# Kernel optimization log

Measured on AMD Instinct MI355X. Metric: run time of the kernel, lower is better.

Reference implementation:

```python
import jax, jax.numpy as jnp
import numpy as np

N_LETTERS = 256
EMBED_DIM = 1024
HIDDEN_DIM = 2048
SEQ_LEN = 4096


def setup_inputs() -> dict:
    key = jax.random.key(0)
    ks = jax.random.split(key, 8)
    s_e = 1.0 / np.sqrt(EMBED_DIM)
    s_h = 1.0 / np.sqrt(HIDDEN_DIM)
    return {
        "input_ids": jax.random.randint(ks[0], (SEQ_LEN,), 0, N_LETTERS, dtype=jnp.int64)
        if jax.config.jax_enable_x64 else jax.random.randint(ks[0], (SEQ_LEN,), 0, N_LETTERS, dtype=jnp.int32),
        "h0": jnp.zeros((1, 1, HIDDEN_DIM), jnp.float32),
        "c0": jnp.zeros((1, 1, HIDDEN_DIM), jnp.float32),
        "W_emb": jax.random.normal(ks[1], (N_LETTERS, EMBED_DIM), jnp.float32),
        "W_ih": jax.random.normal(ks[2], (4 * HIDDEN_DIM, EMBED_DIM), jnp.float32) * s_e,
        "W_hh": jax.random.normal(ks[3], (4 * HIDDEN_DIM, HIDDEN_DIM), jnp.float32) * s_h,
        "b_ih": jnp.zeros((4 * HIDDEN_DIM,), jnp.float32),
        "b_hh": jnp.zeros((4 * HIDDEN_DIM,), jnp.float32),
        "W_out": jax.random.normal(ks[4], (N_LETTERS, HIDDEN_DIM), jnp.float32) * s_h,
        "b_out": jnp.zeros((N_LETTERS,), jnp.float32),
    }


def reference(input_ids, h0, c0, W_emb, W_ih, W_hh, b_ih, b_hh, W_out, b_out):
    H = W_hh.shape[1]
    emb = W_emb[input_ids]                       # [L, E]
    # Precompute the input-side gate projections for all timesteps (batched GEMM).
    x_gates = emb @ W_ih.T + (b_ih + b_hh)       # [L, 4H]

    def step(carry, xg):
        h, c = carry                             # [H], [H]
        gates = xg + W_hh @ h                    # [4H], PyTorch order i,f,g,o
        i = jax.nn.sigmoid(gates[0 * H:1 * H])
        f = jax.nn.sigmoid(gates[1 * H:2 * H])
        g = jnp.tanh(gates[2 * H:3 * H])
        o = jax.nn.sigmoid(gates[3 * H:4 * H])
        c_new = f * c + i * g
        h_new = o * jnp.tanh(c_new)
        return (h_new, c_new), h_new

    (hL, cL), hs = jax.lax.scan(step, (h0[0, 0], c0[0, 0]), x_gates)  # hs: [L, H]
    logits = hs @ W_out.T + b_out                # [L, n_letters]
    # Dropout(p=0.1) is identity in eval mode.
    out = jax.nn.log_softmax(jax.nn.relu(logits), axis=-1)
    return out, hL[None, None, :], cL[None, None, :]
```

## Files before the change

### kernel.cpp

```cpp
#include <hip/hip_runtime.h>
#include <hip/hip_bf16.h>

#define SEQ 4096
#define EMB 1024
#define HID 2048
#define G4  8192
#define NL  256

typedef __attribute__((ext_vector_type(8))) short bf16x8;
typedef __attribute__((ext_vector_type(4))) float f32x4;

static __device__ __forceinline__ unsigned short f2bf(float f) {
    unsigned int x = __builtin_bit_cast(unsigned int, f);
    return (unsigned short)((x + 0x7FFFu + ((x >> 16) & 1u)) >> 16);
}
static __device__ __forceinline__ float bf2f(unsigned short u) {
    return __builtin_bit_cast(float, ((unsigned int)u) << 16);
}
static __device__ __forceinline__ unsigned long long aload(const unsigned long long* p) {
    return __hip_atomic_load(p, __ATOMIC_RELAXED, __HIP_MEMORY_SCOPE_AGENT);
}
static __device__ __forceinline__ float fsigm(float x) {
    return 1.f / (1.f + __expf(-x));
}
static __device__ __forceinline__ float ftanh(float x) {
    return 1.f - 2.f / (__expf(2.f * x) + 1.f);
}

__global__ __launch_bounds__(256) void k_f2b(const float* __restrict__ in,
                                             unsigned short* __restrict__ out, int n) {
    int i = (blockIdx.x * 256 + threadIdx.x) * 4;
    if (i < n) {
        float4 v = *(const float4*)&in[i];
        ushort4 u;
        u.x = f2bf(v.x); u.y = f2bf(v.y); u.z = f2bf(v.z); u.w = f2bf(v.w);
        *(ushort4*)&out[i] = u;
    }
}

__global__ __launch_bounds__(256) void k_emb(const int* __restrict__ ids,
                                             const float* __restrict__ W_emb,
                                             unsigned short* __restrict__ out) {
    int t = blockIdx.x;
    int e0 = threadIdx.x * 4;
    const float4 v = *(const float4*)&W_emb[(size_t)ids[t] * EMB + e0];
    ushort4 u;
    u.x = f2bf(v.x); u.y = f2bf(v.y); u.z = f2bf(v.z); u.w = f2bf(v.w);
    *(ushort4*)&out[(size_t)t * EMB + e0] = u;
}

#define BM 128
#define BN 128
#define BK 32
__global__ __launch_bounds__(256) void k_gemm_bt(
    const unsigned short* __restrict__ A, const unsigned short* __restrict__ B,
    const float* __restrict__ bias1, const float* __restrict__ bias2,
    float* __restrict__ Cf, unsigned short* __restrict__ Cb,
    int M, int N, int K)
{
    __shared__ unsigned short As[BM * BK];
    __shared__ unsigned short Bs[BN * BK];
    const int bm = blockIdx.x * BM;
    const int bn = blockIdx.y * BN;
    const int tid = threadIdx.x;
    const int wave = tid >> 6, lane = tid & 63;
    const int wm = (wave & 1) * 64, wn = (wave >> 1) * 64;
    const int row16 = lane & 15, quad = lane >> 4;

    f32x4 acc[4][4];
#pragma unroll
    for (int i = 0; i < 4; ++i)
#pragma unroll
        for (int j = 0; j < 4; ++j) acc[i][j] = (f32x4){0.f, 0.f, 0.f, 0.f};

    for (int k0 = 0; k0 < K; k0 += BK) {
        __syncthreads();
#pragma unroll
        for (int s = 0; s < 2; ++s) {
            int c = tid + s * 256;
            int r = c >> 2, col = (c & 3) * 8;
            *(uint4*)&As[r * BK + col] = *(const uint4*)&A[(size_t)(bm + r) * K + k0 + col];
            *(uint4*)&Bs[r * BK + col] = *(const uint4*)&B[(size_t)(bn + r) * K + k0 + col];
        }
        __syncthreads();
        bf16x8 af[4], bfr[4];
#pragma unroll
        for (int i = 0; i < 4; ++i) {
            af[i]  = *(const bf16x8*)&As[(wm + i * 16 + row16) * BK + quad * 8];
            bfr[i] = *(const bf16x8*)&Bs[(wn + i * 16 + row16) * BK + quad * 8];
        }
#pragma unroll
        for (int i = 0; i < 4; ++i)
#pragma unroll
            for (int j = 0; j < 4; ++j)
                acc[i][j] = __builtin_amdgcn_mfma_f32_16x16x32_bf16(af[i], bfr[j], acc[i][j], 0, 0, 0);
    }

#pragma unroll
    for (int j = 0; j < 4; ++j) {
        int col = bn + wn + j * 16 + row16;
        float bsum = (bias1 ? bias1[col] : 0.f) + (bias2 ? bias2[col] : 0.f);
#pragma unroll
        for (int i = 0; i < 4; ++i) {
#pragma unroll
            for (int r = 0; r < 4; ++r) {
                int row = bm + wm + i * 16 + quad * 4 + r;
                float v = acc[i][j][r] + bsum;
                if (Cf) Cf[(size_t)row * N + col] = v;
                else    Cb[(size_t)row * N + col] = f2bf(v);
            }
        }
    }
}

#define LSTM_LDS 90112
__global__ __launch_bounds__(1024, 1) void k_lstm(
    const unsigned short* __restrict__ Whhb,
    const unsigned short* __restrict__ xg,
    const float* __restrict__ h0, const float* __restrict__ c0,
    unsigned short* __restrict__ hsb,
    float* __restrict__ outHC,
    unsigned long long* __restrict__ hcomm)
{
    extern __shared__ char smem[];
    float* LDSp = (float*)smem;

    const int b = blockIdx.x, tid = threadIdx.x;
    const int wave = tid >> 6, lane = tid & 63;
    const int sub = lane & 15, quad = lane >> 4;

    const int qa = (sub >> 3), qb = 2 + (sub >> 3), j = sub & 7;
    const unsigned short* wa = Whhb + ((size_t)(qa * HID + b * 8 + j)) * HID + wave * 128 + quad * 8;
    const unsigned short* wb = Whhb + ((size_t)(qb * HID + b * 8 + j)) * HID + wave * 128 + quad * 8;
    bf16x8 afrA[4], afrB[4];
#pragma unroll
    for (int c = 0; c < 4; ++c) {
        afrA[c] = *(const bf16x8*)(wa + c * 32);
        afrB[c] = *(const bf16x8*)(wb + c * 32);
    }

    float creg = 0.f;
    if (tid < 8) creg = c0[b * 8 + tid];

    for (int t = 0; t < SEQ; ++t) {
        float xq0 = 0.f, xq1 = 0.f, xq2 = 0.f, xq3 = 0.f;
        if (wave == 0 && lane < 8) {
            const unsigned short* xr = xg + (size_t)t * G4 + b * 8 + lane;
            xq0 = bf2f(xr[0]);
            xq1 = bf2f(xr[2048]);
            xq2 = bf2f(xr[4096]);
            xq3 = bf2f(xr[6144]);
        }

        f32x4 acc0 = (f32x4){0.f, 0.f, 0.f, 0.f};
        f32x4 acc1 = (f32x4){0.f, 0.f, 0.f, 0.f};

        if (t == 0) {
#pragma unroll
            for (int c = 0; c < 4; ++c) {
                const float* hp = h0 + wave * 128 + c * 32 + quad * 8;
                float4 va = *(const float4*)hp;
                float4 vb = *(const float4*)(hp + 4);
                uint4 d;
                d.x = (unsigned)f2bf(va.x) | ((unsigned)f2bf(va.y) << 16);
                d.y = (unsigned)f2bf(va.z) | ((unsigned)f2bf(va.w) << 16);
                d.z = (unsigned)f2bf(vb.x) | ((unsigned)f2bf(vb.y) << 16);
                d.w = (unsigned)f2bf(vb.z) | ((unsigned)f2bf(vb.w) << 16);
                bf16x8 hf = __builtin_bit_cast(bf16x8, d);
                acc0 = __builtin_amdgcn_mfma_f32_16x16x32_bf16(afrA[c], hf, acc0, 0, 0, 0);
                acc1 = __builtin_amdgcn_mfma_f32_16x16x32_bf16(afrB[c], hf, acc1, 0, 0, 0);
            }
        } else {
            const unsigned long long* src =
                hcomm + (size_t)((t - 1) & 1) * 8192 + (size_t)(b & 7) * 1024 + wave * 64;
            const unsigned tag = (unsigned)t;
            unsigned long long x;
            for (;;) {
                x = aload(&src[lane]);
                if ((unsigned)(x >> 32) == tag) break;
                __builtin_amdgcn_s_sleep(1);
            }
            int myd = (int)(unsigned)x;
#pragma unroll
            for (int c = 0; c < 4; ++c) {
                const int sl = c * 16 + quad * 4;
                uint4 d;
                d.x = (unsigned)__shfl(myd, sl + 0);
                d.y = (unsigned)__shfl(myd, sl + 1);
                d.z = (unsigned)__shfl(myd, sl + 2);
                d.w = (unsigned)__shfl(myd, sl + 3);
                bf16x8 hf = __builtin_bit_cast(bf16x8, d);
                acc0 = __builtin_amdgcn_mfma_f32_16x16x32_bf16(afrA[c], hf, acc0, 0, 0, 0);
                acc1 = __builtin_amdgcn_mfma_f32_16x16x32_bf16(afrB[c], hf, acc1, 0, 0, 0);
            }
        }

        float* P = LDSp + (t & 1) * 640;
        if (sub == 0) {
#pragma unroll
            for (int r = 0; r < 4; ++r) {
                P[(quad * 4 + r) * 20 + wave]      = acc0[r];
                P[(16 + quad * 4 + r) * 20 + wave] = acc1[r];
            }
        }
        __syncthreads();

        if (wave == 0) {
            float g = 0.f;
            if (lane < 32) {
                const float* rp = P + lane * 20;
                f32x4 s = *(const f32x4*)rp;
                s += *(const f32x4*)(rp + 4);
                s += *(const f32x4*)(rp + 8);
                s += *(const f32x4*)(rp + 12);
                g = s[0] + s[1] + s[2] + s[3];
            }
            float gF = __shfl(g, 8 + lane);
            float gG = __shfl(g, 16 + lane);
            float gO = __shfl(g, 24 + lane);
            unsigned hv = 0;
            float cn = 0.f, hn = 0.f;
            if (lane < 8) {
                float gi = g  + xq0;
                float gf = gF + xq1;
                float gg = gG + xq2;
                float go = gO + xq3;
                float i_ = fsigm(gi);
                float f_ = fsigm(gf);
                float g_ = ftanh(gg);
                float o_ = fsigm(go);
                cn = f_ * creg + i_ * g_;
                hn = o_ * ftanh(cn);
                creg = cn;
                hv = (unsigned)f2bf(hn);
            }
            {
                int jj = lane & 3;
                unsigned lo = (unsigned)__shfl((int)hv, 2 * jj);
                unsigned hi = (unsigned)__shfl((int)hv, 2 * jj + 1);
                if (lane < 32) {
                    unsigned long long wrd =
                        (((unsigned long long)(unsigned)(t + 1)) << 32)
                        | (unsigned long long)(lo | (hi << 16));
                    __hip_atomic_store(
                        &hcomm[(size_t)(t & 1) * 8192 + (size_t)(lane >> 2) * 1024 + b * 4 + jj],
                        wrd, __ATOMIC_RELAXED, __HIP_MEMORY_SCOPE_AGENT);
                }
            }
            if (lane < 8) {
                hsb[(size_t)t * HID + b * 8 + lane] = (unsigned short)hv;
                if (t == SEQ - 1) {
                    outHC[b * 8 + lane] = hn;
                    outHC[HID + b * 8 + lane] = cn;
                }
            }
        }
    }
}

__global__ __launch_bounds__(256) void k_softmax(const float* __restrict__ logits,
                                                 float* __restrict__ out) {
    int row = blockIdx.x * 4 + (threadIdx.x >> 6);
    int lane = threadIdx.x & 63;
    const float* Lr = logits + (size_t)row * NL;
    float4 v = *(const float4*)&Lr[lane * 4];
    v.x = fmaxf(v.x, 0.f); v.y = fmaxf(v.y, 0.f);
    v.z = fmaxf(v.z, 0.f); v.w = fmaxf(v.w, 0.f);
    float m = fmaxf(fmaxf(v.x, v.y), fmaxf(v.z, v.w));
#pragma unroll
    for (int off = 32; off > 0; off >>= 1) m = fmaxf(m, __shfl_xor(m, off));
    float e = __expf(v.x - m) + __expf(v.y - m) + __expf(v.z - m) + __expf(v.w - m);
#pragma unroll
    for (int off = 32; off > 0; off >>= 1) e += __shfl_xor(e, off);
    float ls = __logf(e) + m;
    float4 o;
    o.x = v.x - ls; o.y = v.y - ls; o.z = v.z - ls; o.w = v.w - ls;
    *(float4*)&out[(size_t)row * NL + lane * 4] = o;
}

extern "C" void kernel_launch(void* const* d_in, const int* in_sizes, int n_in,
                              void* d_out, int out_size, void* d_ws, size_t ws_size,
                              hipStream_t stream) {
    const int*   ids   = (const int*)d_in[0];
    const float* h0    = (const float*)d_in[1];
    const float* c0    = (const float*)d_in[2];
    const float* W_emb = (const float*)d_in[3];
    const float* W_ih  = (const float*)d_in[4];
    const float* W_hh  = (const float*)d_in[5];
    const float* b_ih  = (const float*)d_in[6];
    const float* b_hh  = (const float*)d_in[7];
    const float* W_out = (const float*)d_in[8];
    const float* b_out = (const float*)d_in[9];
    float* out = (float*)d_out;

    char* ws = (char*)d_ws;
    unsigned short* xg    = (unsigned short*)(ws);
    unsigned short* hsb   = (unsigned short*)(ws + 67108864);
    unsigned short* Wihb  = (unsigned short*)(ws + 83886080);
    unsigned short* embb  = (unsigned short*)(ws + 100663296);
    unsigned short* Woutb = (unsigned short*)(ws + 109051904);
    float*          logit = (float*)(ws + 110100480);
    unsigned short* Whhb  = (unsigned short*)(ws + 114294784);
    unsigned long long* hcomm = (unsigned long long*)(ws + 147849216);

    k_f2b<<<(G4 * EMB / 4 + 255) / 256, 256, 0, stream>>>(W_ih, Wihb, G4 * EMB);
    k_f2b<<<(NL * HID / 4 + 255) / 256, 256, 0, stream>>>(W_out, Woutb, NL * HID);
    k_f2b<<<(G4 * HID / 4 + 255) / 256, 256, 0, stream>>>(W_hh, Whhb, G4 * HID);
    k_emb<<<SEQ, 256, 0, stream>>>(ids, W_emb, embb);

    dim3 g1(SEQ / BM, G4 / BN);
    k_gemm_bt<<<g1, 256, 0, stream>>>(embb, Wihb, b_ih, b_hh, nullptr, xg, SEQ, G4, EMB);

    hipFuncSetAttribute((const void*)k_lstm, hipFuncAttributeMaxDynamicSharedMemorySize, LSTM_LDS);
    k_lstm<<<256, 1024, LSTM_LDS, stream>>>(Whhb, xg, h0, c0, hsb, out + (size_t)SEQ * NL, hcomm);

    dim3 g2(SEQ / BM, NL / BN);
    k_gemm_bt<<<g2, 256, 0, stream>>>(hsb, Woutb, b_out, nullptr, logit, nullptr, SEQ, NL, HID);

    k_softmax<<<SEQ / 4, 256, 0, stream>>>(logit, out);
}
```

Measured before the change: 10.69 ms.

## Halve LSTM grid so each block owns 16 hidden units with full MFMA tiles

The persistent LSTM kernel now runs 128 blocks, each owning 16 hidden units, instead of 256 blocks owning 8. Each wave holds all four gates' W_hh fragments in registers and issues four MFMAs per K-chunk, so every 16-row MFMA tile carries useful rows. The LDS partial-sum layout, the gate reduction, the hcomm broadcast packing and the c/h bookkeeping are reworked to match. Polling is also retuned: non-leader waves sleep before spinning and the spin sleep is longer. The aim is to cut per-step grid-wide synchronisation and polling contention by halving the number of participants. In exchange, each block does twice the matrix work per step and uses more registers.

```diff
diff --git a/kernel.cpp b/kernel.cpp
--- a/kernel.cpp
+++ b/kernel.cpp
@@ -129,31 +129,32 @@
     const int wave = tid >> 6, lane = tid & 63;
     const int sub = lane & 15, quad = lane >> 4;
 
-    const int qa = (sub >> 3), qb = 2 + (sub >> 3), j = sub & 7;
-    const unsigned short* wa = Whhb + ((size_t)(qa * HID + b * 8 + j)) * HID + wave * 128 + quad * 8;
-    const unsigned short* wb = Whhb + ((size_t)(qb * HID + b * 8 + j)) * HID + wave * 128 + quad * 8;
-    bf16x8 afrA[4], afrB[4];
-#pragma unroll
-    for (int c = 0; c < 4; ++c) {
-        afrA[c] = *(const bf16x8*)(wa + c * 32);
-        afrB[c] = *(const bf16x8*)(wb + c * 32);
+    bf16x8 afr[4][4];
+#pragma unroll
+    for (int q = 0; q < 4; ++q) {
+        const unsigned short* wsrc =
+            Whhb + ((size_t)(q * HID + b * 16 + sub)) * HID + wave * 128 + quad * 8;
+#pragma unroll
+        for (int c = 0; c < 4; ++c)
+            afr[q][c] = *(const bf16x8*)(wsrc + c * 32);
     }
 
     float creg = 0.f;
-    if (tid < 8) creg = c0[b * 8 + tid];
+    if (tid < 16) creg = c0[b * 16 + tid];
 
     for (int t = 0; t < SEQ; ++t) {
         float xq0 = 0.f, xq1 = 0.f, xq2 = 0.f, xq3 = 0.f;
-        if (wave == 0 && lane < 8) {
-            const unsigned short* xr = xg + (size_t)t * G4 + b * 8 + lane;
+        if (wave == 0 && lane < 16) {
+            const unsigned short* xr = xg + (size_t)t * G4 + b * 16 + lane;
             xq0 = bf2f(xr[0]);
             xq1 = bf2f(xr[2048]);
             xq2 = bf2f(xr[4096]);
             xq3 = bf2f(xr[6144]);
         }
 
-        f32x4 acc0 = (f32x4){0.f, 0.f, 0.f, 0.f};
-        f32x4 acc1 = (f32x4){0.f, 0.f, 0.f, 0.f};
+        f32x4 acc[4];
+#pragma unroll
+        for (int q = 0; q < 4; ++q) acc[q] = (f32x4){0.f, 0.f, 0.f, 0.f};
 
         if (t == 0) {
 #pragma unroll
@@ -167,18 +168,20 @@
                 d.z = (unsigned)f2bf(vb.x) | ((unsigned)f2bf(vb.y) << 16);
                 d.w = (unsigned)f2bf(vb.z) | ((unsigned)f2bf(vb.w) << 16);
                 bf16x8 hf = __builtin_bit_cast(bf16x8, d);
-                acc0 = __builtin_amdgcn_mfma_f32_16x16x32_bf16(afrA[c], hf, acc0, 0, 0, 0);
-                acc1 = __builtin_amdgcn_mfma_f32_16x16x32_bf16(afrB[c], hf, acc1, 0, 0, 0);
+#pragma unroll
+                for (int q = 0; q < 4; ++q)
+                    acc[q] = __builtin_amdgcn_mfma_f32_16x16x32_bf16(afr[q][c], hf, acc[q], 0, 0, 0);
             }
         } else {
             const unsigned long long* src =
                 hcomm + (size_t)((t - 1) & 1) * 8192 + (size_t)(b & 7) * 1024 + wave * 64;
             const unsigned tag = (unsigned)t;
+            if (wave != 0) __builtin_amdgcn_s_sleep(10);
             unsigned long long x;
             for (;;) {
                 x = aload(&src[lane]);
                 if ((unsigned)(x >> 32) == tag) break;
-                __builtin_amdgcn_s_sleep(1);
+                __builtin_amdgcn_s_sleep(2);
             }
             int myd = (int)(unsigned)x;
 #pragma unroll
@@ -190,37 +193,33 @@
                 d.z = (unsigned)__shfl(myd, sl + 2);
                 d.w = (unsigned)__shfl(myd, sl + 3);
                 bf16x8 hf = __builtin_bit_cast(bf16x8, d);
-                acc0 = __builtin_amdgcn_mfma_f32_16x16x32_bf16(afrA[c], hf, acc0, 0, 0, 0);
-                acc1 = __builtin_amdgcn_mfma_f32_16x16x32_bf16(afrB[c], hf, acc1, 0, 0, 0);
-            }
-        }
-
-        float* P = LDSp + (t & 1) * 640;
+#pragma unroll
+                for (int q = 0; q < 4; ++q)
+                    acc[q] = __builtin_amdgcn_mfma_f32_16x16x32_bf16(afr[q][c], hf, acc[q], 0, 0, 0);
+            }
+        }
+
+        float* P = LDSp + (t & 1) * 1100;
         if (sub == 0) {
 #pragma unroll
-            for (int r = 0; r < 4; ++r) {
-                P[(quad * 4 + r) * 20 + wave]      = acc0[r];
-                P[(16 + quad * 4 + r) * 20 + wave] = acc1[r];
-            }
+            for (int q = 0; q < 4; ++q)
+#pragma unroll
+                for (int r = 0; r < 4; ++r)
+                    P[(q * 16 + quad * 4 + r) * 17 + wave] = acc[q][r];
         }
         __syncthreads();
 
         if (wave == 0) {
+            const float* rp = P + lane * 17;
             float g = 0.f;
-            if (lane < 32) {
-                const float* rp = P + lane * 20;
-                f32x4 s = *(const f32x4*)rp;
-                s += *(const f32x4*)(rp + 4);
-                s += *(const f32x4*)(rp + 8);
-                s += *(const f32x4*)(rp + 12);
-                g = s[0] + s[1] + s[2] + s[3];
-            }
-            float gF = __shfl(g, 8 + lane);
-            float gG = __shfl(g, 16 + lane);
-            float gO = __shfl(g, 24 + lane);
+#pragma unroll
+            for (int i = 0; i < 16; ++i) g += rp[i];
+            float gF = __shfl(g, lane + 16);
+            float gG = __shfl(g, lane + 32);
+            float gO = __shfl(g, lane + 48);
             unsigned hv = 0;
             float cn = 0.f, hn = 0.f;
-            if (lane < 8) {
+            if (lane < 16) {
                 float gi = g  + xq0;
                 float gf = gF + xq1;
                 float gg = gG + xq2;
@@ -235,23 +234,21 @@
                 hv = (unsigned)f2bf(hn);
             }
             {
-                int jj = lane & 3;
-                unsigned lo = (unsigned)__shfl((int)hv, 2 * jj);
-                unsigned hi = (unsigned)__shfl((int)hv, 2 * jj + 1);
-                if (lane < 32) {
-                    unsigned long long wrd =
-                        (((unsigned long long)(unsigned)(t + 1)) << 32)
-                        | (unsigned long long)(lo | (hi << 16));
-                    __hip_atomic_store(
-                        &hcomm[(size_t)(t & 1) * 8192 + (size_t)(lane >> 2) * 1024 + b * 4 + jj],
-                        wrd, __ATOMIC_RELAXED, __HIP_MEMORY_SCOPE_AGENT);
-                }
-            }
-            if (lane < 8) {
-                hsb[(size_t)t * HID + b * 8 + lane] = (unsigned short)hv;
+                int j8 = lane & 7;
+                unsigned lo = (unsigned)__shfl((int)hv, 2 * j8);
+                unsigned hi = (unsigned)__shfl((int)hv, 2 * j8 + 1);
+                unsigned long long wrd =
+                    (((unsigned long long)(unsigned)(t + 1)) << 32)
+                    | (unsigned long long)(lo | (hi << 16));
+                __hip_atomic_store(
+                    &hcomm[(size_t)(t & 1) * 8192 + (size_t)(lane >> 3) * 1024 + b * 8 + j8],
+                    wrd, __ATOMIC_RELAXED, __HIP_MEMORY_SCOPE_AGENT);
+            }
+            if (lane < 16) {
+                hsb[(size_t)t * HID + b * 16 + lane] = (unsigned short)hv;
                 if (t == SEQ - 1) {
-                    outHC[b * 8 + lane] = hn;
-                    outHC[HID + b * 8 + lane] = cn;
+                    outHC[b * 16 + lane] = hn;
+                    outHC[HID + b * 16 + lane] = cn;
                 }
             }
         }
@@ -312,7 +309,7 @@
     k_gemm_bt<<<g1, 256, 0, stream>>>(embb, Wihb, b_ih, b_hh, nullptr, xg, SEQ, G4, EMB);
 
     hipFuncSetAttribute((const void*)k_lstm, hipFuncAttributeMaxDynamicSharedMemorySize, LSTM_LDS);
-    k_lstm<<<256, 1024, LSTM_LDS, stream>>>(Whhb, xg, h0, c0, hsb, out + (size_t)SEQ * NL, hcomm);
+    k_lstm<<<128, 1024, LSTM_LDS, stream>>>(Whhb, xg, h0, c0, hsb, out + (size_t)SEQ * NL, hcomm);
 
     dim3 g2(SEQ / BM, NL / BN);
     k_gemm_bt<<<g2, 256, 0, stream>>>(hsb, Woutb, b_out, nullptr, logit, nullptr, SEQ, NL, HID);
```

After: 10.82 ms. No clear change (+1.2%).
